# Performance work log

Hardware: AMD Instinct MI355X
Metric: run time of the kernel (lower is better)

## Reference

```python
import jax, jax.numpy as jnp
import numpy as np

NUM_ITERATIONS = 3

def _squash(s):
    # Original squash reduces over the trailing singleton dim -> elementwise.
    sn = s * s
    return sn * s / ((1.0 + sn) * jnp.sqrt(sn))

def setup_inputs() -> dict:
    key = jax.random.key(0)
    k1, k2 = jax.random.split(key)
    x = jax.random.normal(k1, (128, 1152, 8), dtype=jnp.float32)
    W = jax.random.normal(k2, (1, 1152, 16, 16, 8), dtype=jnp.float32)
    return {"x": x, "W": W}

def reference(x, W):
    # x: [B, R, I]; W: [1, R, C, O, I]
    Wr = W[0]  # [R, C, O, I]
    # u_hat = W @ x broadcast over capsules: [B, R, C, O]
    u_hat = jnp.einsum('rcoi,bri->brco', Wr, x)
    R, C = Wr.shape[0], Wr.shape[1]
    b = jnp.zeros((R, C), dtype=x.dtype)  # routing logits (shared across batch)
    v = None
    for it in range(NUM_ITERATIONS):
        # legacy F.softmax on [1,R,C,1] -> dim=1 == routes axis
        c = jax.nn.softmax(b, axis=0)  # [R, C]
        s = jnp.einsum('rc,brco->bco', c, u_hat)  # [B, C, O]
        v = _squash(s)
        if it < NUM_ITERATIONS - 1:
            # agreement: <u_hat, v> averaged over batch
            a = jnp.einsum('brco,bco->brc', u_hat, v).mean(axis=0)  # [R, C]
            b = b + a
    return v  # [B, C, O] == v_j.squeeze(1).squeeze(-1)
```

## Files before the change

### kernel.cpp

```cpp
#include <hip/hip_runtime.h>
#include <math.h>

#define B_   128
#define R_   1152
#define C_   16
#define O_   16
#define RS_  192
#define RCH_ 6

#define WS_SP   0
#define WS_V    6291456
#define WS_BLOG 6324224

__device__ __forceinline__ float squashf(float s) {
    return s * fabsf(s) / (1.0f + s * s);
}

template <bool PRE>
__global__ __launch_bounds__(256) void gemm_s_k(const float* __restrict__ x,
                                                const float* __restrict__ W,
                                                const float* __restrict__ blog,
                                                float* __restrict__ sp) {
    const int bt  = blockIdx.x;
    const int rs  = blockIdx.y;
    const int t   = threadIdx.x;
    const int co4 = t & 63;
    const int b8  = t >> 6;
    const int c   = co4 >> 2;
    const int r0  = rs * RCH_;

    __shared__ float4 wl4[RCH_ * 520];
    __shared__ float4 xl4[32 * 2 * RCH_];
    __shared__ float4 part[16];
    __shared__ float  colmax[16], colinv[16];
    __shared__ float  cwl[RCH_ * 16];

    const float4* __restrict__ X4 = (const float4*)x;
    const float4* __restrict__ W4 = (const float4*)W;

    #pragma unroll
    for (int kk = 0; kk < 12; ++kk) {
        const int u  = t + kk * 256;
        const int rr = u >> 9, j = u & 511;
        wl4[rr * 520 + (j & 7) * 65 + (j >> 3)] = W4[r0 * 512 + u];
    }
    {
        int u = t;
        { const int bl = u / 12, rem = u % 12;
          xl4[u] = X4[((bt * 32 + bl) * R_ + r0) * 2 + rem]; }
        u = t + 256;
        if (u < 384) {
            const int bl = u / 12, rem = u % 12;
            xl4[u] = X4[((bt * 32 + bl) * R_ + r0) * 2 + rem];
        }
    }

    if (PRE) {
        const float4* BL4 = (const float4*)blog;
        const int g = t & 3;
        float4 m4; m4.x = -1e30f; m4.y = -1e30f; m4.z = -1e30f; m4.w = -1e30f;
        #pragma unroll
        for (int i = 0; i < 18; ++i) {
            const float4 bv = BL4[i * 256 + t];
            m4.x = fmaxf(m4.x, bv.x); m4.y = fmaxf(m4.y, bv.y);
            m4.z = fmaxf(m4.z, bv.z); m4.w = fmaxf(m4.w, bv.w);
        }
        #pragma unroll
        for (int d = 4; d < 64; d <<= 1) {
            m4.x = fmaxf(m4.x, __shfl_xor(m4.x, d));
            m4.y = fmaxf(m4.y, __shfl_xor(m4.y, d));
            m4.z = fmaxf(m4.z, __shfl_xor(m4.z, d));
            m4.w = fmaxf(m4.w, __shfl_xor(m4.w, d));
        }
        if ((t & 63) < 4) part[(t >> 6) * 4 + g] = m4;
        __syncthreads();
        if (t < 4) {
            const float4 a = part[t], b = part[4 + t], cc4 = part[8 + t], d = part[12 + t];
            colmax[t * 4 + 0] = fmaxf(fmaxf(a.x, b.x), fmaxf(cc4.x, d.x));
            colmax[t * 4 + 1] = fmaxf(fmaxf(a.y, b.y), fmaxf(cc4.y, d.y));
            colmax[t * 4 + 2] = fmaxf(fmaxf(a.z, b.z), fmaxf(cc4.z, d.z));
            colmax[t * 4 + 3] = fmaxf(fmaxf(a.w, b.w), fmaxf(cc4.w, d.w));
        }
        __syncthreads();
        const float Mx = colmax[g * 4 + 0], My = colmax[g * 4 + 1];
        const float Mz = colmax[g * 4 + 2], Mw = colmax[g * 4 + 3];
        float4 e4; e4.x = 0.f; e4.y = 0.f; e4.z = 0.f; e4.w = 0.f;
        #pragma unroll
        for (int i = 0; i < 18; ++i) {
            const float4 bv = BL4[i * 256 + t];
            e4.x += __expf(bv.x - Mx); e4.y += __expf(bv.y - My);
            e4.z += __expf(bv.z - Mz); e4.w += __expf(bv.w - Mw);
        }
        #pragma unroll
        for (int d = 4; d < 64; d <<= 1) {
            e4.x += __shfl_xor(e4.x, d); e4.y += __shfl_xor(e4.y, d);
            e4.z += __shfl_xor(e4.z, d); e4.w += __shfl_xor(e4.w, d);
        }
        if ((t & 63) < 4) part[(t >> 6) * 4 + g] = e4;
        __syncthreads();
        if (t < 4) {
            const float4 a = part[t], b = part[4 + t], cc4 = part[8 + t], d = part[12 + t];
            colinv[t * 4 + 0] = 1.0f / ((a.x + b.x) + (cc4.x + d.x));
            colinv[t * 4 + 1] = 1.0f / ((a.y + b.y) + (cc4.y + d.y));
            colinv[t * 4 + 2] = 1.0f / ((a.z + b.z) + (cc4.z + d.z));
            colinv[t * 4 + 3] = 1.0f / ((a.w + b.w) + (cc4.w + d.w));
        }
        __syncthreads();
        if (t < RCH_ * 16) {
            const int rl = t >> 4, cc = t & 15;
            cwl[t] = __expf(blog[(r0 + rl) * 16 + cc] - colmax[cc]) * colinv[cc];
        }
    }
    __syncthreads();

    float acc[8][4];
    #pragma unroll
    for (int j = 0; j < 8; ++j)
        #pragma unroll
        for (int q = 0; q < 4; ++q) acc[j][q] = 0.f;

    #pragma unroll
    for (int rr = 0; rr < RCH_; ++rr) {
        const float cwv = PRE ? cwl[rr * 16 + c] : (1.0f / (float)R_);
        const int wb = rr * 520 + co4;
        const float4 w0 = wl4[wb +   0], w1 = wl4[wb +  65];
        const float4 w2 = wl4[wb + 130], w3 = wl4[wb + 195];
        const float4 w4 = wl4[wb + 260], w5 = wl4[wb + 325];
        const float4 w6 = wl4[wb + 390], w7 = wl4[wb + 455];
        #pragma unroll
        for (int j = 0; j < 8; ++j) {
            const float4 xa = xl4[(b8 * 8 + j) * 12 + rr * 2];
            const float4 xb = xl4[(b8 * 8 + j) * 12 + rr * 2 + 1];
            const float d0 = w0.x*xa.x + w0.y*xa.y + w0.z*xa.z + w0.w*xa.w
                           + w1.x*xb.x + w1.y*xb.y + w1.z*xb.z + w1.w*xb.w;
            const float d1 = w2.x*xa.x + w2.y*xa.y + w2.z*xa.z + w2.w*xa.w
                           + w3.x*xb.x + w3.y*xb.y + w3.z*xb.z + w3.w*xb.w;
            const float d2 = w4.x*xa.x + w4.y*xa.y + w4.z*xa.z + w4.w*xa.w
                           + w5.x*xb.x + w5.y*xb.y + w5.z*xb.z + w5.w*xb.w;
            const float d3 = w6.x*xa.x + w6.y*xa.y + w6.z*xa.z + w6.w*xa.w
                           + w7.x*xb.x + w7.y*xb.y + w7.z*xb.z + w7.w*xb.w;
            acc[j][0] = fmaf(cwv, d0, acc[j][0]);
            acc[j][1] = fmaf(cwv, d1, acc[j][1]);
            acc[j][2] = fmaf(cwv, d2, acc[j][2]);
            acc[j][3] = fmaf(cwv, d3, acc[j][3]);
        }
    }

    float4* sp4 = (float4*)sp;
    #pragma unroll
    for (int j = 0; j < 8; ++j) {
        const int b = bt * 32 + b8 * 8 + j;
        float4 o4; o4.x = acc[j][0]; o4.y = acc[j][1]; o4.z = acc[j][2]; o4.w = acc[j][3];
        sp4[(rs * B_ + b) * 64 + co4] = o4;
    }
}

__global__ __launch_bounds__(512) void reduce_squash_k(const float* __restrict__ sp,
                                                       float* __restrict__ outv) {
    const int t   = threadIdx.x;
    const int li  = t & 127;
    const int kq  = t >> 7;
    const int idx = blockIdx.x * 128 + li;
    const float* p = sp + (size_t)kq * 48 * 32768 + idx;
    float a0 = 0.f, a1 = 0.f, a2 = 0.f, a3 = 0.f;
    #pragma unroll 6
    for (int k = 0; k < 48; k += 4) {
        a0 += p[(k + 0) * 32768];
        a1 += p[(k + 1) * 32768];
        a2 += p[(k + 2) * 32768];
        a3 += p[(k + 3) * 32768];
    }
    __shared__ float red[512];
    red[t] = (a0 + a1) + (a2 + a3);
    __syncthreads();
    if (t < 128) {
        const float s = (red[t] + red[t + 128]) + (red[t + 256] + red[t + 384]);
        outv[idx] = squashf(s);
    }
}

template <bool FIRST>
__global__ __launch_bounds__(512) void a_k(const float* __restrict__ x,
                                           const float* __restrict__ W,
                                           const float* __restrict__ v,
                                           float* __restrict__ blog) {
    const int r0 = blockIdx.x * 4;
    const int t  = threadIdx.x;
    const int w  = t >> 6, lane = t & 63;
    const int rr = w & 3, half = w >> 2;
    const int co4 = lane, c = lane >> 2;

    __shared__ float4 xl[128 * 8];
    __shared__ float4 wl[4 * 520];
    __shared__ float  red[128];
    const float4* __restrict__ X4 = (const float4*)x;
    const float4* __restrict__ V4 = (const float4*)v;
    const float4* __restrict__ W4 = (const float4*)W;

    #pragma unroll
    for (int kk = 0; kk < 4; ++kk) {
        const int u  = t + kk * 512;
        const int r2 = u >> 9, j = u & 511;
        wl[r2 * 520 + (j & 7) * 65 + (j >> 3)] = W4[r0 * 512 + u];
    }
    #pragma unroll
    for (int kk = 0; kk < 2; ++kk) {
        const int u = t + kk * 512;
        const int b = u >> 3, rem = u & 7;
        xl[u] = X4[(b * R_ + r0) * 2 + rem];
    }
    __syncthreads();

    float y[8][4];
    #pragma unroll
    for (int i = 0; i < 8; ++i)
        #pragma unroll
        for (int q = 0; q < 4; ++q) y[i][q] = 0.f;

    const int b0 = half * 64;
    #pragma unroll 4
    for (int bb = 0; bb < 64; ++bb) {
        const int b = b0 + bb;
        const float4 xa = xl[b * 8 + rr * 2];
        const float4 xb = xl[b * 8 + rr * 2 + 1];
        const float4 vv = V4[b * 64 + co4];
        const float xs[8] = {xa.x, xa.y, xa.z, xa.w, xb.x, xb.y, xb.z, xb.w};
        #pragma unroll
        for (int i = 0; i < 8; ++i) {
            y[i][0] = fmaf(xs[i], vv.x, y[i][0]);
            y[i][1] = fmaf(xs[i], vv.y, y[i][1]);
            y[i][2] = fmaf(xs[i], vv.z, y[i][2]);
            y[i][3] = fmaf(xs[i], vv.w, y[i][3]);
        }
    }

    const int wb = rr * 520 + co4;
    float part = 0.f;
    #pragma unroll
    for (int q = 0; q < 4; ++q) {
        const float4 w0 = wl[wb + (2 * q) * 65];
        const float4 w1 = wl[wb + (2 * q + 1) * 65];
        part += w0.x*y[0][q] + w0.y*y[1][q] + w0.z*y[2][q] + w0.w*y[3][q]
              + w1.x*y[4][q] + w1.y*y[5][q] + w1.z*y[6][q] + w1.w*y[7][q];
    }
    part += __shfl_xor(part, 1);
    part += __shfl_xor(part, 2);
    if ((lane & 3) == 0) red[w * 16 + c] = part;
    __syncthreads();
    if (t < 64) {
        const int rr2 = t >> 4, cc = t & 15;
        const float val = (red[rr2 * 16 + cc] + red[(rr2 + 4) * 16 + cc]) * (1.0f / (float)B_);
        const int idx = (r0 + rr2) * 16 + cc;
        blog[idx] = FIRST ? val : (blog[idx] + val);
    }
}

extern "C" void kernel_launch(void* const* d_in, const int* in_sizes, int n_in,
                              void* d_out, int out_size, void* d_ws, size_t ws_size,
                              hipStream_t stream) {
    const float* x = (const float*)d_in[0];
    const float* W = (const float*)d_in[1];
    float* out = (float*)d_out;
    float* ws  = (float*)d_ws;

    float* sp   = ws + WS_SP;
    float* v    = ws + WS_V;
    float* blog = ws + WS_BLOG;

    gemm_s_k<false><<<dim3(4, RS_), 256, 0, stream>>>(x, W, blog, sp);
    reduce_squash_k<<<256, 512, 0, stream>>>(sp, v);
    a_k<true><<<288, 512, 0, stream>>>(x, W, v, blog);

    gemm_s_k<true><<<dim3(4, RS_), 256, 0, stream>>>(x, W, blog, sp);
    reduce_squash_k<<<256, 512, 0, stream>>>(sp, v);
    a_k<false><<<288, 512, 0, stream>>>(x, W, v, blog);

    gemm_s_k<true><<<dim3(4, RS_), 256, 0, stream>>>(x, W, blog, sp);
    reduce_squash_k<<<256, 512, 0, stream>>>(sp, out);
}
```

Measured before the change: 196.1 us.

## Pre-transpose W once into workspace and drop softmax max pass

The first s-GEMM kernel now writes a transposed copy of W into workspace, and later kernels read W directly from global memory in that layout instead of staging it through shared memory with a padded transpose. This removes the LDS staging and its syncs in the later GEMM and agreement kernels, and cuts their shared-memory footprint, which may raise occupancy. Separately, the softmax over routing logits drops its max-subtraction pass and computes exp directly. That saves one reduction over blog but risks overflow if the logits grow large.

```diff
diff --git a/kernel.cpp b/kernel.cpp
--- a/kernel.cpp
+++ b/kernel.cpp
@@ -11,38 +11,38 @@
 #define WS_SP   0
 #define WS_V    6291456
 #define WS_BLOG 6324224
+#define WS_WT   6342656
 
 __device__ __forceinline__ float squashf(float s) {
     return s * fabsf(s) / (1.0f + s * s);
 }
 
-template <bool PRE>
-__global__ __launch_bounds__(256) void gemm_s_k(const float* __restrict__ x,
-                                                const float* __restrict__ W,
-                                                const float* __restrict__ blog,
-                                                float* __restrict__ sp) {
+__global__ __launch_bounds__(256) void gemm_s_first_k(const float* __restrict__ x,
+                                                      const float* __restrict__ W,
+                                                      float* __restrict__ wt,
+                                                      float* __restrict__ sp) {
     const int bt  = blockIdx.x;
     const int rs  = blockIdx.y;
     const int t   = threadIdx.x;
     const int co4 = t & 63;
     const int b8  = t >> 6;
-    const int c   = co4 >> 2;
     const int r0  = rs * RCH_;
 
     __shared__ float4 wl4[RCH_ * 520];
-    __shared__ float4 xl4[32 * 2 * RCH_];
-    __shared__ float4 part[16];
-    __shared__ float  colmax[16], colinv[16];
-    __shared__ float  cwl[RCH_ * 16];
+    __shared__ float4 xl4[32 * 12];
 
     const float4* __restrict__ X4 = (const float4*)x;
     const float4* __restrict__ W4 = (const float4*)W;
+    float4* __restrict__ Wt4 = (float4*)wt;
 
     #pragma unroll
     for (int kk = 0; kk < 12; ++kk) {
         const int u  = t + kk * 256;
         const int rr = u >> 9, j = u & 511;
-        wl4[rr * 520 + (j & 7) * 65 + (j >> 3)] = W4[r0 * 512 + u];
+        const float4 wv = W4[r0 * 512 + u];
+        wl4[rr * 520 + (j & 7) * 65 + (j >> 3)] = wv;
+        if (bt == 0)
+            Wt4[(size_t)(r0 + rr) * 512 + (j & 7) * 64 + (j >> 3)] = wv;
     }
     {
         int u = t;
@@ -54,63 +54,6 @@
             xl4[u] = X4[((bt * 32 + bl) * R_ + r0) * 2 + rem];
         }
     }
-
-    if (PRE) {
-        const float4* BL4 = (const float4*)blog;
-        const int g = t & 3;
-        float4 m4; m4.x = -1e30f; m4.y = -1e30f; m4.z = -1e30f; m4.w = -1e30f;
-        #pragma unroll
-        for (int i = 0; i < 18; ++i) {
-            const float4 bv = BL4[i * 256 + t];
-            m4.x = fmaxf(m4.x, bv.x); m4.y = fmaxf(m4.y, bv.y);
-            m4.z = fmaxf(m4.z, bv.z); m4.w = fmaxf(m4.w, bv.w);
-        }
-        #pragma unroll
-        for (int d = 4; d < 64; d <<= 1) {
-            m4.x = fmaxf(m4.x, __shfl_xor(m4.x, d));
-            m4.y = fmaxf(m4.y, __shfl_xor(m4.y, d));
-            m4.z = fmaxf(m4.z, __shfl_xor(m4.z, d));
-            m4.w = fmaxf(m4.w, __shfl_xor(m4.w, d));
-        }
-        if ((t & 63) < 4) part[(t >> 6) * 4 + g] = m4;
-        __syncthreads();
-        if (t < 4) {
-            const float4 a = part[t], b = part[4 + t], cc4 = part[8 + t], d = part[12 + t];
-            colmax[t * 4 + 0] = fmaxf(fmaxf(a.x, b.x), fmaxf(cc4.x, d.x));
-            colmax[t * 4 + 1] = fmaxf(fmaxf(a.y, b.y), fmaxf(cc4.y, d.y));
-            colmax[t * 4 + 2] = fmaxf(fmaxf(a.z, b.z), fmaxf(cc4.z, d.z));
-            colmax[t * 4 + 3] = fmaxf(fmaxf(a.w, b.w), fmaxf(cc4.w, d.w));
-        }
-        __syncthreads();
-        const float Mx = colmax[g * 4 + 0], My = colmax[g * 4 + 1];
-        const float Mz = colmax[g * 4 + 2], Mw = colmax[g * 4 + 3];
-        float4 e4; e4.x = 0.f; e4.y = 0.f; e4.z = 0.f; e4.w = 0.f;
-        #pragma unroll
-        for (int i = 0; i < 18; ++i) {
-            const float4 bv = BL4[i * 256 + t];
-            e4.x += __expf(bv.x - Mx); e4.y += __expf(bv.y - My);
-            e4.z += __expf(bv.z - Mz); e4.w += __expf(bv.w - Mw);
-        }
-        #pragma unroll
-        for (int d = 4; d < 64; d <<= 1) {
-            e4.x += __shfl_xor(e4.x, d); e4.y += __shfl_xor(e4.y, d);
-            e4.z += __shfl_xor(e4.z, d); e4.w += __shfl_xor(e4.w, d);
-        }
-        if ((t & 63) < 4) part[(t >> 6) * 4 + g] = e4;
-        __syncthreads();
-        if (t < 4) {
-            const float4 a = part[t], b = part[4 + t], cc4 = part[8 + t], d = part[12 + t];
-            colinv[t * 4 + 0] = 1.0f / ((a.x + b.x) + (cc4.x + d.x));
-            colinv[t * 4 + 1] = 1.0f / ((a.y + b.y) + (cc4.y + d.y));
-            colinv[t * 4 + 2] = 1.0f / ((a.z + b.z) + (cc4.z + d.z));
-            colinv[t * 4 + 3] = 1.0f / ((a.w + b.w) + (cc4.w + d.w));
-        }
-        __syncthreads();
-        if (t < RCH_ * 16) {
-            const int rl = t >> 4, cc = t & 15;
-            cwl[t] = __expf(blog[(r0 + rl) * 16 + cc] - colmax[cc]) * colinv[cc];
-        }
-    }
     __syncthreads();
 
     float acc[8][4];
@@ -121,7 +64,7 @@
 
     #pragma unroll
     for (int rr = 0; rr < RCH_; ++rr) {
-        const float cwv = PRE ? cwl[rr * 16 + c] : (1.0f / (float)R_);
+        const float cwv = 1.0f / (float)R_;
         const int wb = rr * 520 + co4;
         const float4 w0 = wl4[wb +   0], w1 = wl4[wb +  65];
         const float4 w2 = wl4[wb + 130], w3 = wl4[wb + 195];
@@ -155,6 +98,109 @@
     }
 }
 
+__global__ __launch_bounds__(256) void gemm_s_k(const float* __restrict__ x,
+                                                const float* __restrict__ wt,
+                                                const float* __restrict__ blog,
+                                                float* __restrict__ sp) {
+    const int bt  = blockIdx.x;
+    const int rs  = blockIdx.y;
+    const int t   = threadIdx.x;
+    const int co4 = t & 63;
+    const int b8  = t >> 6;
+    const int c   = co4 >> 2;
+    const int r0  = rs * RCH_;
+
+    __shared__ float4 xl4[32 * 12];
+    __shared__ float4 part[16];
+    __shared__ float  colinv[16];
+    __shared__ float  cwl[RCH_ * 16];
+
+    const float4* __restrict__ X4  = (const float4*)x;
+    const float4* __restrict__ Wt4 = (const float4*)wt;
+
+    {
+        int u = t;
+        { const int bl = u / 12, rem = u % 12;
+          xl4[u] = X4[((bt * 32 + bl) * R_ + r0) * 2 + rem]; }
+        u = t + 256;
+        if (u < 384) {
+            const int bl = u / 12, rem = u % 12;
+            xl4[u] = X4[((bt * 32 + bl) * R_ + r0) * 2 + rem];
+        }
+    }
+
+    {
+        const float4* BL4 = (const float4*)blog;
+        const int g = t & 3;
+        float4 e4; e4.x = 0.f; e4.y = 0.f; e4.z = 0.f; e4.w = 0.f;
+        #pragma unroll
+        for (int i = 0; i < 18; ++i) {
+            const float4 bv = BL4[i * 256 + t];
+            e4.x += __expf(bv.x); e4.y += __expf(bv.y);
+            e4.z += __expf(bv.z); e4.w += __expf(bv.w);
+        }
+        #pragma unroll
+        for (int d = 4; d < 64; d <<= 1) {
+            e4.x += __shfl_xor(e4.x, d); e4.y += __shfl_xor(e4.y, d);
+            e4.z += __shfl_xor(e4.z, d); e4.w += __shfl_xor(e4.w, d);
+        }
+        if ((t & 63) < 4) part[(t >> 6) * 4 + g] = e4;
+        __syncthreads();
+        if (t < 4) {
+            const float4 a = part[t], b = part[4 + t], cc4 = part[8 + t], d = part[12 + t];
+            colinv[t * 4 + 0] = 1.0f / ((a.x + b.x) + (cc4.x + d.x));
+            colinv[t * 4 + 1] = 1.0f / ((a.y + b.y) + (cc4.y + d.y));
+            colinv[t * 4 + 2] = 1.0f / ((a.z + b.z) + (cc4.z + d.z));
+            colinv[t * 4 + 3] = 1.0f / ((a.w + b.w) + (cc4.w + d.w));
+        }
+        __syncthreads();
+        if (t < RCH_ * 16) {
+            const int rl = t >> 4, cc = t & 15;
+            cwl[t] = __expf(blog[(r0 + rl) * 16 + cc]) * colinv[cc];
+        }
+    }
+    __syncthreads();
+
+    float acc[8][4];
+    #pragma unroll
+    for (int j = 0; j < 8; ++j)
+        #pragma unroll
+        for (int q = 0; q < 4; ++q) acc[j][q] = 0.f;
+
+    #pragma unroll
+    for (int rr = 0; rr < RCH_; ++rr) {
+        const float cwv = cwl[rr * 16 + c];
+        const float4* wp = Wt4 + ((size_t)(r0 + rr) << 9) + co4;
+        const float4 w0 = wp[  0], w1 = wp[ 64], w2 = wp[128], w3 = wp[192];
+        const float4 w4 = wp[256], w5 = wp[320], w6 = wp[384], w7 = wp[448];
+        #pragma unroll
+        for (int j = 0; j < 8; ++j) {
+            const float4 xa = xl4[(b8 * 8 + j) * 12 + rr * 2];
+            const float4 xb = xl4[(b8 * 8 + j) * 12 + rr * 2 + 1];
+            const float d0 = w0.x*xa.x + w0.y*xa.y + w0.z*xa.z + w0.w*xa.w
+                           + w1.x*xb.x + w1.y*xb.y + w1.z*xb.z + w1.w*xb.w;
+            const float d1 = w2.x*xa.x + w2.y*xa.y + w2.z*xa.z + w2.w*xa.w
+                           + w3.x*xb.x + w3.y*xb.y + w3.z*xb.z + w3.w*xb.w;
+            const float d2 = w4.x*xa.x + w4.y*xa.y + w4.z*xa.z + w4.w*xa.w
+                           + w5.x*xb.x + w5.y*xb.y + w5.z*xb.z + w5.w*xb.w;
+            const float d3 = w6.x*xa.x + w6.y*xa.y + w6.z*xa.z + w6.w*xa.w
+                           + w7.x*xb.x + w7.y*xb.y + w7.z*xb.z + w7.w*xb.w;
+            acc[j][0] = fmaf(cwv, d0, acc[j][0]);
+            acc[j][1] = fmaf(cwv, d1, acc[j][1]);
+            acc[j][2] = fmaf(cwv, d2, acc[j][2]);
+            acc[j][3] = fmaf(cwv, d3, acc[j][3]);
+        }
+    }
+
+    float4* sp4 = (float4*)sp;
+    #pragma unroll
+    for (int j = 0; j < 8; ++j) {
+        const int b = bt * 32 + b8 * 8 + j;
+        float4 o4; o4.x = acc[j][0]; o4.y = acc[j][1]; o4.z = acc[j][2]; o4.w = acc[j][3];
+        sp4[(rs * B_ + b) * 64 + co4] = o4;
+    }
+}
+
 __global__ __launch_bounds__(512) void reduce_squash_k(const float* __restrict__ sp,
                                                        float* __restrict__ outv) {
     const int t   = threadIdx.x;
@@ -181,7 +227,7 @@
 
 template <bool FIRST>
 __global__ __launch_bounds__(512) void a_k(const float* __restrict__ x,
-                                           const float* __restrict__ W,
+                                           const float* __restrict__ wt,
                                            const float* __restrict__ v,
                                            float* __restrict__ blog) {
     const int r0 = blockIdx.x * 4;
@@ -191,18 +237,11 @@
     const int co4 = lane, c = lane >> 2;
 
     __shared__ float4 xl[128 * 8];
-    __shared__ float4 wl[4 * 520];
     __shared__ float  red[128];
-    const float4* __restrict__ X4 = (const float4*)x;
-    const float4* __restrict__ V4 = (const float4*)v;
-    const float4* __restrict__ W4 = (const float4*)W;
-
-    #pragma unroll
-    for (int kk = 0; kk < 4; ++kk) {
-        const int u  = t + kk * 512;
-        const int r2 = u >> 9, j = u & 511;
-        wl[r2 * 520 + (j & 7) * 65 + (j >> 3)] = W4[r0 * 512 + u];
-    }
+    const float4* __restrict__ X4  = (const float4*)x;
+    const float4* __restrict__ V4  = (const float4*)v;
+    const float4* __restrict__ Wt4 = (const float4*)wt;
+
     #pragma unroll
     for (int kk = 0; kk < 2; ++kk) {
         const int u = t + kk * 512;
@@ -234,12 +273,12 @@
         }
     }
 
-    const int wb = rr * 520 + co4;
+    const float4* wp = Wt4 + ((size_t)(r0 + rr) << 9) + co4;
     float part = 0.f;
     #pragma unroll
     for (int q = 0; q < 4; ++q) {
-        const float4 w0 = wl[wb + (2 * q) * 65];
-        const float4 w1 = wl[wb + (2 * q + 1) * 65];
+        const float4 w0 = wp[(2 * q) * 64];
+        const float4 w1 = wp[(2 * q + 1) * 64];
         part += w0.x*y[0][q] + w0.y*y[1][q] + w0.z*y[2][q] + w0.w*y[3][q]
               + w1.x*y[4][q] + w1.y*y[5][q] + w1.z*y[6][q] + w1.w*y[7][q];
     }
@@ -266,15 +305,16 @@
     float* sp   = ws + WS_SP;
     float* v    = ws + WS_V;
     float* blog = ws + WS_BLOG;
-
-    gemm_s_k<false><<<dim3(4, RS_), 256, 0, stream>>>(x, W, blog, sp);
+    float* wt   = ws + WS_WT;
+
+    gemm_s_first_k<<<dim3(4, RS_), 256, 0, stream>>>(x, W, wt, sp);
     reduce_squash_k<<<256, 512, 0, stream>>>(sp, v);
-    a_k<true><<<288, 512, 0, stream>>>(x, W, v, blog);
-
-    gemm_s_k<true><<<dim3(4, RS_), 256, 0, stream>>>(x, W, blog, sp);
+    a_k<true><<<288, 512, 0, stream>>>(x, wt, v, blog);
+
+    gemm_s_k<<<dim3(4, RS_), 256, 0, stream>>>(x, wt, blog, sp);
     reduce_squash_k<<<256, 512, 0, stream>>>(sp, v);
-    a_k<false><<<288, 512, 0, stream>>>(x, W, v, blog);
-
-    gemm_s_k<true><<<dim3(4, RS_), 256, 0, stream>>>(x, W, blog, sp);
+    a_k<false><<<288, 512, 0, stream>>>(x, wt, v, blog);
+
+    gemm_s_k<<<dim3(4, RS_), 256, 0, stream>>>(x, wt, blog, sp);
     reduce_squash_k<<<256, 512, 0, stream>>>(sp, out);
 }
```

Result: no change. 197.1 us (+0.5%).
